# Kernel tuning notes

Hardware: AMD Instinct MI355X
Metric: run time of the kernel (lower is better)

## Reference

```python
import jax, jax.numpy as jnp
import numpy as np

EPS = 1e-4          # ReEig epsilon buffer
IN_SIZE = 4096      # input SPD matrix is IN_SIZE x IN_SIZE
HID = 5             # hard-coded bottleneck in RiemSPD
OUT_SIZE = 2048     # output SPD matrix is OUT_SIZE x OUT_SIZE


def _orthogonal(key, rows, cols):
    # mimic nn.init.orthogonal_: semi-orthogonal (rows, cols) matrix
    n, m = max(rows, cols), min(rows, cols)
    a = jax.random.normal(key, (n, m), dtype=jnp.float32)
    q, _ = jnp.linalg.qr(a)
    q = q[:, :m]
    return q if rows >= cols else q.T


def bimap(x, w):
    # BiMap.forward: W^T @ X @ W
    return w.T @ (x @ w)


def rectify(x):
    # Rectify.forward: SVD, clip singular values at EPS, rebuild u diag(s) u^T
    u, s, _ = jnp.linalg.svd(x)
    s = jnp.maximum(s, EPS)
    return (u * s[None, :]) @ u.T


def setup_inputs() -> dict:
    key = jax.random.key(0)
    k1, k2, k3 = jax.random.split(key, 3)
    X = jax.random.normal(k1, (1, IN_SIZE, IN_SIZE), dtype=jnp.float32)
    W1 = _orthogonal(k2, IN_SIZE, HID)   # encoder BiMap weight (in_size, 5)
    W2 = _orthogonal(k3, HID, OUT_SIZE)  # decoder BiMap weight (5, out_size)
    return {"X": X, "W1": W1, "W2": W2}


def reference(X, W1, W2):
    x = X[0]                       # squeeze(0): (IN_SIZE, IN_SIZE)
    y = rectify(bimap(x, W1))      # encoder: (5, 5)
    z = rectify(bimap(y, W2))      # decoder: (OUT_SIZE, OUT_SIZE)
    return z
```

## Files before the change

kernel.cpp:

```cpp
#include <hip/hip_runtime.h>
#include <math.h>

static constexpr int N   = 4096;
static constexpr int H   = 5;
static constexpr int NO  = 2048;
static constexpr float FEPS = 1e-4f;
static constexpr int NJC  = 4;
static constexpr int NIG  = 128;
static constexpr int RPB  = N / NIG;
static constexpr int NBLK = NIG * NJC;
static constexpr int NCON = 256;
static constexpr int NR   = NO / NCON;

#if __has_builtin(__builtin_amdgcn_rcpf)
__device__ __forceinline__ float frcp(float x) { return __builtin_amdgcn_rcpf(x); }
#else
__device__ __forceinline__ float frcp(float x) { return 1.0f / x; }
#endif
#if __has_builtin(__builtin_amdgcn_rsqf)
__device__ __forceinline__ float frsq(float x) { return __builtin_amdgcn_rsqf(x); }
#else
__device__ __forceinline__ float frsq(float x) { return 1.0f / sqrtf(x); }
#endif

__device__ __forceinline__ float wave_reduce(float v) {
#pragma unroll
    for (int o = 32; o > 0; o >>= 1) v += __shfl_down(v, o, 64);
    return v;
}

__global__ __launch_bounds__(256) void k_xw1(const float* __restrict__ X,
                                             const float* __restrict__ W1,
                                             float* __restrict__ Mp) {
    const int b   = blockIdx.x;
    const int ig  = b >> 2;
    const int jcb = b & 3;
    const int t   = threadIdx.x;
    const int j4  = jcb * 256 + t;
    const float4* W14 = reinterpret_cast<const float4*>(W1);

    float wf[20];
    {
        const float4 f0 = W14[5 * j4 + 0];
        const float4 f1 = W14[5 * j4 + 1];
        const float4 f2 = W14[5 * j4 + 2];
        const float4 f3 = W14[5 * j4 + 3];
        const float4 f4 = W14[5 * j4 + 4];
        wf[0]=f0.x;  wf[1]=f0.y;  wf[2]=f0.z;  wf[3]=f0.w;
        wf[4]=f1.x;  wf[5]=f1.y;  wf[6]=f1.z;  wf[7]=f1.w;
        wf[8]=f2.x;  wf[9]=f2.y;  wf[10]=f2.z; wf[11]=f2.w;
        wf[12]=f3.x; wf[13]=f3.y; wf[14]=f3.z; wf[15]=f3.w;
        wf[16]=f4.x; wf[17]=f4.y; wf[18]=f4.z; wf[19]=f4.w;
    }

    float pm[H][H];
#pragma unroll
    for (int a = 0; a < H; ++a)
#pragma unroll
        for (int bb = 0; bb < H; ++bb) pm[a][bb] = 0.f;

    const int i0 = ig * RPB;
#pragma unroll 4
    for (int r = 0; r < RPB; ++r) {
        const float4 x = reinterpret_cast<const float4*>(
                             X + (size_t)(i0 + r) * N)[j4];
        float t5[H];
#pragma unroll
        for (int a = 0; a < H; ++a)
            t5[a] = x.x * wf[a]      + x.y * wf[5 + a]
                  + x.z * wf[10 + a] + x.w * wf[15 + a];
        float w1r[H];
#pragma unroll
        for (int a = 0; a < H; ++a) w1r[a] = W1[(size_t)(i0 + r) * H + a];
#pragma unroll
        for (int a = 0; a < H; ++a)
#pragma unroll
            for (int bb = 0; bb < H; ++bb) pm[a][bb] += w1r[a] * t5[bb];
    }

    __shared__ float sm[4][25];
    {
        const int lane = t & 63, wv = t >> 6;
#pragma unroll
        for (int a = 0; a < H; ++a)
#pragma unroll
            for (int bb = 0; bb < H; ++bb) {
                const float v = wave_reduce(pm[a][bb]);
                if (lane == 0) sm[wv][a * H + bb] = v;
            }
    }
    __syncthreads();
    if (t < 25)
        Mp[b * 25 + t] = sm[0][t] + sm[1][t] + sm[2][t] + sm[3][t];
}

#define JROT(p, q)                                                            \
    {                                                                         \
        const float apq = __shfl(a, (p) * 5 + (q), 64);                       \
        const float app = __shfl(a, (p) * 5 + (p), 64);                       \
        const float aqq = __shfl(a, (q) * 5 + (q), 64);                       \
        const bool  skip =                                                    \
            (apq * apq) <= (1e-26f * (app * app + aqq * aqq) + 1e-38f);       \
        const float theta = (aqq - app) * frcp(2.0f * apq);                   \
        const float tden  = fabsf(theta) + sqrtf(theta * theta + 1.0f);       \
        const float ttv   = ((theta >= 0.0f) ? 1.0f : -1.0f) * frcp(tden);    \
        float cc = frsq(ttv * ttv + 1.0f);                                    \
        float ss = ttv * cc;                                                  \
        cc = skip ? 1.0f : cc;                                                \
        ss = skip ? 0.0f : ss;                                                \
        {                                                                     \
            const int  pr   = ((r == (p)) ? (q) : ((r == (q)) ? (p) : r));    \
            const float prt = __shfl(a, pr * 5 + c, 64);                      \
            a = (r == (p)) ? (cc * a - ss * prt)                              \
                           : ((r == (q)) ? (ss * prt + cc * a) : a);          \
        }                                                                     \
        {                                                                     \
            const int  pc   = ((c == (p)) ? (q) : ((c == (q)) ? (p) : c));    \
            const float prt = __shfl(a, r * 5 + pc, 64);                      \
            a = (c == (p)) ? (cc * a - ss * prt)                              \
                           : ((c == (q)) ? (ss * prt + cc * a) : a);          \
            const float urt = __shfl(u, r * 5 + pc, 64);                      \
            u = (c == (p)) ? (cc * u - ss * urt)                              \
                           : ((c == (q)) ? (ss * urt + cc * u) : u);          \
        }                                                                     \
    }

__global__ __launch_bounds__(256) void k_out(const float* __restrict__ Mp,
                                             const float* __restrict__ W2,
                                             float* __restrict__ Z) {
    __shared__ float sred[10][26];
    __shared__ float Msum[25];
    __shared__ float ys[25];
    const int t = threadIdx.x;
    const int i0 = blockIdx.x * NR;

    float4 w2j[2][H];
    float  wcol[NR][H];
#pragma unroll
    for (int hh = 0; hh < 2; ++hh) {
        const int jj = (hh * 256 + t) * 4;
#pragma unroll
        for (int m = 0; m < H; ++m)
            w2j[hh][m] = *reinterpret_cast<const float4*>(W2 + (size_t)m * NO + jj);
    }
#pragma unroll
    for (int r = 0; r < NR; ++r)
#pragma unroll
        for (int k = 0; k < H; ++k) wcol[r][k] = W2[(size_t)k * NO + i0 + r];

    if (t < 250) {
        const int e = t % 25, g = t / 25;
        float s = 0.f;
#pragma unroll 8
        for (int p = g; p < NBLK; p += 10) s += Mp[p * 25 + e];
        sred[g][e] = s;
    }
    __syncthreads();
    if (t < 25) {
        float s = 0.f;
#pragma unroll
        for (int g = 0; g < 10; ++g) s += sred[g][t];
        Msum[t] = s;
    }
    __syncthreads();

    if (t < 64) {
        const int r = t / 5, c = t % 5;
        const float m = (t < 25) ? Msum[t] : 0.f;
        float a = 0.f;
#pragma unroll
        for (int k = 0; k < H; ++k)
            a += __shfl(m, r * 5 + k, 64) * __shfl(m, c * 5 + k, 64);
        float u = (t < 25 && r == c) ? 1.0f : 0.0f;

        for (int sweep = 0; sweep < 6; ++sweep) {
            JROT(0, 1) JROT(0, 2) JROT(0, 3) JROT(0, 4) JROT(1, 2)
            JROT(1, 3) JROT(1, 4) JROT(2, 3) JROT(2, 4) JROT(3, 4)
        }

        const float ev = fmaxf(sqrtf(fmaxf(a, 0.0f)), FEPS);
        float yv = 0.f;
#pragma unroll
        for (int k = 0; k < H; ++k) {
            const float evk = __shfl(ev, 6 * k, 64);
            const float urk = __shfl(u, r * 5 + k, 64);
            const float uck = __shfl(u, c * 5 + k, 64);
            yv += evk * urk * uck;
        }
        if (t < 25) ys[t] = yv - ((r == c) ? FEPS : 0.f);
    }
    __syncthreads();

    float cmat[NR][H];
#pragma unroll
    for (int r = 0; r < NR; ++r)
#pragma unroll
        for (int m = 0; m < H; ++m) {
            float s = 0.f;
#pragma unroll
            for (int k = 0; k < H; ++k) s += wcol[r][k] * ys[k * H + m];
            cmat[r][m] = s;
        }

#pragma unroll
    for (int hh = 0; hh < 2; ++hh) {
        const int jj = (hh * 256 + t) * 4;
#pragma unroll
        for (int r = 0; r < NR; ++r) {
            const int i = i0 + r;
            float zx = 0.f, zy = 0.f, zz = 0.f, zw = 0.f;
#pragma unroll
            for (int m = 0; m < H; ++m) {
                const float cm = cmat[r][m];
                zx += cm * w2j[hh][m].x;
                zy += cm * w2j[hh][m].y;
                zz += cm * w2j[hh][m].z;
                zw += cm * w2j[hh][m].w;
            }
            if (i >= jj && i < jj + 4) {
                if      (i == jj + 0) zx += FEPS;
                else if (i == jj + 1) zy += FEPS;
                else if (i == jj + 2) zz += FEPS;
                else                  zw += FEPS;
            }
            *reinterpret_cast<float4*>(Z + (size_t)i * NO + jj) =
                make_float4(zx, zy, zz, zw);
        }
    }
}

extern "C" void kernel_launch(void* const* d_in, const int* in_sizes, int n_in,
                              void* d_out, int out_size, void* d_ws, size_t ws_size,
                              hipStream_t stream) {
    const float* X  = (const float*)d_in[0];
    const float* W1 = (const float*)d_in[1];
    const float* W2 = (const float*)d_in[2];
    float* out = (float*)d_out;
    float* ws  = (float*)d_ws;

    float* Mp = ws;

    hipLaunchKernelGGL(k_xw1, dim3(NBLK), dim3(256), 0, stream, X, W1, Mp);
    hipLaunchKernelGGL(k_out, dim3(NCON), dim3(256), 0, stream, Mp, W2, out);
}
```

Before: 40.71 us.

## Double-buffer X row chunks into LDS with async global-to-LDS loads

The encoder X·W1 kernel now stages X in chunks of 8 rows into a double-buffered shared-memory tile using global_load_lds. The next chunk is prefetched while the current one is consumed from LDS. The aim is to keep more memory requests in flight and overlap the streaming of X with the FMA work. The cost is 64KB of LDS per block, which limits occupancy, plus a barrier per chunk. The change also depends on the barrier waiting for the async loads to land.

```diff
diff --git a/kernel.cpp b/kernel.cpp
--- a/kernel.cpp
+++ b/kernel.cpp
@@ -9,6 +9,9 @@
 static constexpr int NIG  = 128;
 static constexpr int RPB  = N / NIG;
 static constexpr int NBLK = NIG * NJC;
+static constexpr int CR   = 8;
+static constexpr int NCH  = RPB / CR;
+static constexpr int CF4  = CR * 256;
 static constexpr int NCON = 256;
 static constexpr int NR   = NO / NCON;
 
@@ -32,12 +35,25 @@
 __global__ __launch_bounds__(256) void k_xw1(const float* __restrict__ X,
                                              const float* __restrict__ W1,
                                              float* __restrict__ Mp) {
-    const int b   = blockIdx.x;
-    const int ig  = b >> 2;
-    const int jcb = b & 3;
-    const int t   = threadIdx.x;
-    const int j4  = jcb * 256 + t;
+    const int b    = blockIdx.x;
+    const int ig   = b >> 2;
+    const int jcb  = b & 3;
+    const int t    = threadIdx.x;
+    const int w    = t >> 6, lane = t & 63;
+    const int j4   = jcb * 256 + t;
     const float4* W14 = reinterpret_cast<const float4*>(W1);
+    const float4* X4  = reinterpret_cast<const float4*>(X);
+    const int i0   = ig * RPB;
+
+    __shared__ float4 xs[2][CF4];
+
+#pragma unroll
+    for (int k = 0; k < 8; ++k) {
+        const int c = w * 512 + k * 64 + lane;
+        const float4* gp = X4 + (size_t)(i0 + (c >> 8)) * (N / 4)
+                              + jcb * 256 + (c & 255);
+        __builtin_amdgcn_global_load_lds(gp, &xs[0][w * 512 + k * 64], 16, 0, 0);
+    }
 
     float wf[20];
     {
@@ -59,34 +75,48 @@
 #pragma unroll
         for (int bb = 0; bb < H; ++bb) pm[a][bb] = 0.f;
 
-    const int i0 = ig * RPB;
-#pragma unroll 4
-    for (int r = 0; r < RPB; ++r) {
-        const float4 x = reinterpret_cast<const float4*>(
-                             X + (size_t)(i0 + r) * N)[j4];
-        float t5[H];
-#pragma unroll
-        for (int a = 0; a < H; ++a)
-            t5[a] = x.x * wf[a]      + x.y * wf[5 + a]
-                  + x.z * wf[10 + a] + x.w * wf[15 + a];
-        float w1r[H];
-#pragma unroll
-        for (int a = 0; a < H; ++a) w1r[a] = W1[(size_t)(i0 + r) * H + a];
-#pragma unroll
-        for (int a = 0; a < H; ++a)
-#pragma unroll
-            for (int bb = 0; bb < H; ++bb) pm[a][bb] += w1r[a] * t5[bb];
+    __syncthreads();
+
+#pragma unroll
+    for (int ch = 0; ch < NCH; ++ch) {
+        if (ch < NCH - 1) {
+#pragma unroll
+            for (int k = 0; k < 8; ++k) {
+                const int c = w * 512 + k * 64 + lane;
+                const float4* gp = X4 + (size_t)(i0 + (ch + 1) * CR + (c >> 8)) * (N / 4)
+                                      + jcb * 256 + (c & 255);
+                __builtin_amdgcn_global_load_lds(gp, &xs[(ch + 1) & 1][w * 512 + k * 64],
+                                                 16, 0, 0);
+            }
+        }
+#pragma unroll
+        for (int r = 0; r < CR; ++r) {
+            const int row = i0 + ch * CR + r;
+            const float4 x = xs[ch & 1][r * 256 + t];
+            float t5[H];
+#pragma unroll
+            for (int a = 0; a < H; ++a)
+                t5[a] = x.x * wf[a]      + x.y * wf[5 + a]
+                      + x.z * wf[10 + a] + x.w * wf[15 + a];
+            float w1r[H];
+#pragma unroll
+            for (int a = 0; a < H; ++a) w1r[a] = W1[(size_t)row * H + a];
+#pragma unroll
+            for (int a = 0; a < H; ++a)
+#pragma unroll
+                for (int bb = 0; bb < H; ++bb) pm[a][bb] += w1r[a] * t5[bb];
+        }
+        __syncthreads();
     }
 
     __shared__ float sm[4][25];
     {
-        const int lane = t & 63, wv = t >> 6;
 #pragma unroll
         for (int a = 0; a < H; ++a)
 #pragma unroll
             for (int bb = 0; bb < H; ++bb) {
                 const float v = wave_reduce(pm[a][bb]);
-                if (lane == 0) sm[wv][a * H + bb] = v;
+                if (lane == 0) sm[w][a * H + bb] = v;
             }
     }
     __syncthreads();
```

New measurement: 68.95 us. +69.4%, slower.
